# Optimization experiments

Hardware: AMD Instinct MI355X
Metric: run time of the kernel (lower is better)

Reference implementation:

```python
import jax, jax.numpy as jnp
import numpy as np

NUM_MID = 10   # hard-coded num_mid_nodes in HiPool.__init__
NUM_HIGH = 5   # ceil(10 / 2)


def map_low_to_high(num_low, num_high):
    # eye(num_high) repeat_interleaved by ceil(low/high) rows, truncated to num_low
    # == one-hot of i // edges_per_high
    edges_per_high = -(-num_low // num_high)
    return jax.nn.one_hot(jnp.arange(num_low) // edges_per_high, num_high,
                          dtype=jnp.float32)  # [low, high]


def cluster_attention(x, mapping, att):
    # x: [s, d], mapping: [s, m], att: [d, d]
    mid = mapping.T @ x                              # [m, d]
    scores = (mid @ att) @ x.T                       # [m, s]
    scores = scores * (1.0 - mapping).T              # zero (not -inf) own-cluster entries, as in source
    scores = jax.nn.softmax(scores, axis=1)
    return scores @ x + mid                          # [m, d]


def dense_gcn(x, adj, W, b):
    # torch_geometric DenseGCNConv with add_loop=True
    n = adj.shape[0]
    i = jnp.arange(n)
    adj = adj.at[i, i].set(1.0)
    deg = jnp.clip(jnp.sum(adj, axis=-1), 1.0, None) ** -0.5
    adj = deg[:, None] * adj * deg[None, :]
    return adj @ (x @ W) + b


def setup_inputs() -> dict:
    key = jax.random.key(0)
    ks = jax.random.split(key, 8)
    S, D, H = 8192, 768, 768
    return {
        "x": jax.random.normal(ks[0], (S, D), dtype=jnp.float32),
        "adjacency_matrix": jax.random.uniform(ks[1], (S, S), dtype=jnp.float32),
        "att_low_mid": jax.random.normal(ks[2], (D, D), dtype=jnp.float32) * 0.04,  # xavier_normal-ish
        "conv1_w": jax.random.normal(ks[3], (D, H), dtype=jnp.float32) * 0.04,
        "conv1_b": jnp.zeros((H,), dtype=jnp.float32),
        "att_mid_high": jax.random.normal(ks[4], (H, H), dtype=jnp.float32) * 0.04,
        "conv2_w": jax.random.normal(ks[5], (H, H), dtype=jnp.float32) * 0.04,
        "conv2_b": jnp.zeros((H,), dtype=jnp.float32),
    }


def reference(x, adjacency_matrix, att_low_mid, conv1_w, conv1_b,
              att_mid_high, conv2_w, conv2_b):
    s = x.shape[0]
    m1 = map_low_to_high(s, NUM_MID)                         # [s, 10]
    mid_adj = m1.T @ adjacency_matrix @ m1                   # [10, 10]
    mid_rep = cluster_attention(x, m1, att_low_mid)          # [10, d]
    x_mid = jax.nn.relu(dense_gcn(mid_rep, mid_adj, conv1_w, conv1_b))
    # F.dropout(...)[0]: dropout treated as identity (eval); [0] just dropped the batch dim
    m2 = map_low_to_high(NUM_MID, NUM_HIGH)                  # [10, 5]
    high_adj = m2.T @ mid_adj @ m2                           # [5, 5]
    high_rep = cluster_attention(x_mid, m2, att_mid_high)    # [5, h]
    out = jax.nn.relu(dense_gcn(high_rep, high_adj, conv2_w, conv2_b))
    return out.mean(axis=0)                                  # [h]
```

## Files before the change

### kernel.cpp

```cpp
#include <hip/hip_runtime.h>

constexpr int S    = 8192;
constexpr int D    = 768;
constexpr int NMID = 10;
constexpr int EPH  = 820;

constexpr int PART_ADJ = 0;
constexpr int PART_MID = 3200;
constexpr int OFF_ZB   = 64640;
constexpr int OFF_MATT = 64640;
constexpr int OFF_Y1   = 72320;
constexpr int OFF_Z2   = 80000;
constexpr int OFF_Y2   = 83840;
constexpr int ZERO_N   = 23040;
constexpr int OFF_MID  = 87680;
constexpr int OFF_XMID = 95360;
constexpr int OFF_SC   = 103040;
constexpr int OFF_SCB  = 184960;
constexpr int OFF_PVP  = 190080;

__device__ __forceinline__ void adj_partial(const float* __restrict__ A,
                                            float* __restrict__ ws, int item) {
    __shared__ float wred[4];
    int p = item >> 5, s = item & 31;
    int i = p / 10, j = p % 10;
    int r0 = i * EPH, nr = min(EPH, S - r0);
    int c0 = j * EPH, nc = min(EPH, S - c0);
    int rs0 = r0 + (nr * s) / 32, rs1 = r0 + (nr * (s + 1)) / 32;
    int nc4 = nc >> 2;
    int tid = threadIdx.x;
    float acc = 0.f;
    for (int r = rs0; r < rs1; ++r) {
        const float4* row = (const float4*)(A + (size_t)r * S + c0);
        if (tid < nc4) {
            float4 v = row[tid];
            acc += (v.x + v.y) + (v.z + v.w);
        }
    }
#pragma unroll
    for (int off = 32; off > 0; off >>= 1) acc += __shfl_down(acc, off, 64);
    int ln = tid & 63, wv = tid >> 6;
    if (ln == 0) wred[wv] = acc;
    __syncthreads();
    if (tid == 0) ws[PART_ADJ + item] = (wred[0] + wred[1]) + (wred[2] + wred[3]);
}

__device__ __forceinline__ void mid_partial(const float* __restrict__ x,
                                            float* __restrict__ ws, int item) {
    int cl = item / 24, rem = item % 24;
    int cc = rem >> 3, sp = rem & 7;
    int r0 = cl * EPH, nr = min(EPH, S - r0);
    int rs0 = r0 + (nr * sp) / 8, rs1 = r0 + (nr * (sp + 1)) / 8;
    int c = cc * 256 + threadIdx.x;
    float acc = 0.f;
    for (int r = rs0; r < rs1; ++r) acc += x[(size_t)r * D + c];
    ws[PART_MID + (sp * NMID + cl) * D + c] = acc;
}

template <int NR>
__device__ __forceinline__ void mm_core(const float* __restrict__ W,
                                        const float* mi,
                                        float* __restrict__ out, int kb) {
    int c = threadIdx.x;
    float a0[NR], a1[NR], a2[NR];
#pragma unroll
    for (int i = 0; i < NR; ++i) { a0[i] = 0.f; a1[i] = 0.f; a2[i] = 0.f; }
    for (int kk = 0; kk < 16; ++kk) {
        const float* wr = W + (size_t)(kb + kk) * D;
        float w0 = wr[c], w1 = wr[c + 256], w2 = wr[c + 512];
#pragma unroll
        for (int i = 0; i < NR; ++i) {
            float m = mi[i * 16 + kk];
            a0[i] += m * w0; a1[i] += m * w1; a2[i] += m * w2;
        }
    }
#pragma unroll
    for (int i = 0; i < NR; ++i) {
        atomicAdd(&out[i * D + c],       a0[i]);
        atomicAdd(&out[i * D + c + 256], a1[i]);
        atomicAdd(&out[i * D + c + 512], a2[i]);
    }
}

__global__ __launch_bounds__(256) void k1(const float* __restrict__ A,
                                          const float* __restrict__ x,
                                          float* __restrict__ ws) {
    int bx = blockIdx.x;
    if (bx < 800) adj_partial(A, ws, bx);
    else if (bx < 1040) mid_partial(x, ws, bx - 800);
    else {
        int b = bx - 1040;
        for (int t = b * 256 + threadIdx.x; t < ZERO_N; t += 16 * 256)
            ws[OFF_ZB + t] = 0.f;
    }
}

__global__ __launch_bounds__(256) void k2(const float* __restrict__ attL,
                                          const float* __restrict__ A,
                                          float* __restrict__ ws) {
    int bx = blockIdx.x;
    if (bx >= 48) { adj_partial(A, ws, 800 + bx - 48); return; }
    __shared__ float mi[160];
    int kb = bx * 16, tid = threadIdx.x;
    if (tid < 160) {
        int cl = tid >> 4, k = tid & 15;
        float s = 0.f;
#pragma unroll
        for (int sp = 0; sp < 8; ++sp)
            s += ws[PART_MID + (sp * NMID + cl) * D + kb + k];
        mi[tid] = s;
        ws[OFF_MID + cl * D + kb + k] = s;
    }
    __syncthreads();
    mm_core<10>(attL, mi, ws + OFF_MATT, kb);
}

__global__ __launch_bounds__(256) void k3(const float* __restrict__ x,
                                          const float* __restrict__ A,
                                          float* __restrict__ ws) {
    int bx = blockIdx.x;
    if (bx >= 256) { adj_partial(A, ws, 1600 + bx - 256); return; }
    __shared__ float ma[NMID * D];
    __shared__ float scl[32 * NMID];
    int tid = threadIdx.x;
    for (int t = tid; t < NMID * D; t += 256) ma[t] = ws[OFF_MATT + t];
    __syncthreads();
    const float4* maf = (const float4*)ma;
    const float4* x4  = (const float4*)x;
    int wave = tid >> 6, ln = tid & 63;
    int rbase = bx * 32 + wave * 8;
    for (int rr = 0; rr < 8; ++rr) {
        int r = rbase + rr;
        float4 v0 = x4[(size_t)r * 192 + ln];
        float4 v1 = x4[(size_t)r * 192 + 64 + ln];
        float4 v2 = x4[(size_t)r * 192 + 128 + ln];
        int rc = r / EPH;
#pragma unroll
        for (int i = 0; i < NMID; ++i) {
            float4 m0 = maf[i * 192 + ln];
            float4 m1 = maf[i * 192 + 64 + ln];
            float4 m2 = maf[i * 192 + 128 + ln];
            float p = m0.x * v0.x + m0.y * v0.y + m0.z * v0.z + m0.w * v0.w
                    + m1.x * v1.x + m1.y * v1.y + m1.z * v1.z + m1.w * v1.w
                    + m2.x * v2.x + m2.y * v2.y + m2.z * v2.z + m2.w * v2.w;
#pragma unroll
            for (int off = 32; off > 0; off >>= 1) p += __shfl_down(p, off, 64);
            if (ln == 0) {
                float v = (rc == i) ? 0.f : p;
                ws[OFF_SC + r * NMID + i] = v;
                scl[(wave * 8 + rr) * NMID + i] = v;
            }
        }
    }
    __syncthreads();
    if (tid < NMID) {
        float m = -1e30f;
        for (int r = 0; r < 32; ++r) m = fmaxf(m, scl[r * NMID + tid]);
        float s = 0.f;
        for (int r = 0; r < 32; ++r) s += expf(scl[r * NMID + tid] - m);
        ws[OFF_SCB + bx * 20 + tid * 2]     = m;
        ws[OFF_SCB + bx * 20 + tid * 2 + 1] = s;
    }
}

__global__ __launch_bounds__(256) void k4(const float* __restrict__ x,
                                          const float* __restrict__ A,
                                          float* __restrict__ ws) {
    int bx = blockIdx.x;
    if (bx >= 64) { adj_partial(A, ws, 2200 + bx - 64); return; }
    __shared__ float lm[160], ls[160], Mi[10], Inv[10], p[128 * NMID];
    int tid = threadIdx.x;
    if (tid < 160) {
        int i = tid >> 4, seg = tid & 15;
        float m = -1e30f;
        for (int b = seg * 16; b < seg * 16 + 16; ++b)
            m = fmaxf(m, ws[OFF_SCB + b * 20 + i * 2]);
        float s = 0.f;
        for (int b = seg * 16; b < seg * 16 + 16; ++b)
            s += ws[OFF_SCB + b * 20 + i * 2 + 1] *
                 expf(ws[OFF_SCB + b * 20 + i * 2] - m);
        lm[tid] = m; ls[tid] = s;
    }
    __syncthreads();
    if (tid < NMID) {
        float M = -1e30f;
        for (int g = 0; g < 16; ++g) M = fmaxf(M, lm[tid * 16 + g]);
        float Ssum = 0.f;
        for (int g = 0; g < 16; ++g) Ssum += ls[tid * 16 + g] * expf(lm[tid * 16 + g] - M);
        Mi[tid] = M; Inv[tid] = 1.f / Ssum;
    }
    __syncthreads();
    int r0 = bx * 128;
    for (int t = tid; t < 128 * NMID; t += 256) {
        int i = t % NMID;
        p[t] = expf(ws[OFF_SC + r0 * NMID + t] - Mi[i]) * Inv[i];
    }
    __syncthreads();
    float a0[NMID], a1[NMID], a2[NMID];
#pragma unroll
    for (int i = 0; i < NMID; ++i) { a0[i] = 0.f; a1[i] = 0.f; a2[i] = 0.f; }
    for (int r = 0; r < 128; ++r) {
        const float* xr = x + (size_t)(r0 + r) * D;
        float x0 = xr[tid], x1 = xr[tid + 256], x2 = xr[tid + 512];
#pragma unroll
        for (int i = 0; i < NMID; ++i) {
            float pv = p[r * NMID + i];
            a0[i] += pv * x0; a1[i] += pv * x1; a2[i] += pv * x2;
        }
    }
#pragma unroll
    for (int i = 0; i < NMID; ++i) {
        float* base = ws + OFF_PVP + (bx * NMID + i) * D;
        base[tid]       = a0[i];
        base[tid + 256] = a1[i];
        base[tid + 512] = a2[i];
    }
}

__global__ __launch_bounds__(256) void k5(const float* __restrict__ W1,
                                          const float* __restrict__ A,
                                          float* __restrict__ ws) {
    int bx = blockIdx.x;
    if (bx >= 48) { adj_partial(A, ws, 2800 + bx - 48); return; }
    __shared__ float mi[160];
    int kb = bx * 16, tid = threadIdx.x;
    if (tid < 160) {
        int cl = tid >> 4, k = tid & 15;
        float s = ws[OFF_MID + cl * D + kb + k];
        for (int b = 0; b < 64; ++b)
            s += ws[OFF_PVP + (b * NMID + cl) * D + kb + k];
        mi[tid] = s;
    }
    __syncthreads();
    mm_core<10>(W1, mi, ws + OFF_Y1, kb);
}

__global__ __launch_bounds__(256) void k6(const float* __restrict__ attH,
                                          const float* __restrict__ b1,
                                          float* __restrict__ ws) {
    __shared__ float aa[100], dg[10], NM[100], xml[160], mi[80];
    int tid = threadIdx.x;
    if (tid < 100) {
        float s = 0.f;
#pragma unroll
        for (int sp = 0; sp < 32; ++sp) s += ws[PART_ADJ + tid * 32 + sp];
        aa[tid] = s;
    }
    __syncthreads();
    if (tid < 10) {
        float s = 0.f;
#pragma unroll
        for (int j = 0; j < 10; ++j) s += (tid == j) ? 1.0f : aa[tid * 10 + j];
        dg[tid] = 1.0f / sqrtf(fmaxf(s, 1.0f));
    }
    __syncthreads();
    if (tid < 100) {
        int i = tid / 10, j = tid % 10;
        NM[tid] = dg[i] * ((i == j) ? 1.0f : aa[tid]) * dg[j];
    }
    __syncthreads();
    int kb = blockIdx.x * 16;
    if (tid < 160) {
        int i = tid >> 4, c = kb + (tid & 15);
        float s = b1[c];
#pragma unroll
        for (int j = 0; j < 10; ++j) s += NM[i * 10 + j] * ws[OFF_Y1 + j * D + c];
        float xm = fmaxf(s, 0.f);
        ws[OFF_XMID + i * D + c] = xm;
        xml[tid] = xm;
    }
    __syncthreads();
    if (tid < 80) {
        int a = tid >> 4, k = tid & 15;
        mi[tid] = xml[(2 * a) * 16 + k] + xml[(2 * a + 1) * 16 + k];
    }
    __syncthreads();
    mm_core<5>(attH, mi, ws + OFF_Z2, kb);
}

__global__ __launch_bounds__(256) void k7(const float* __restrict__ W2,
                                          float* __restrict__ ws) {
    __shared__ float s2[64], P2[50], mi[80];
    int tid = threadIdx.x, wv = tid >> 6, ln = tid & 63;
    for (int pp = wv; pp < 50; pp += 4) {
        int i = pp / 10, r = pp % 10;
        const float4* za = (const float4*)(ws + OFF_Z2 + i * D);
        const float4* xa = (const float4*)(ws + OFF_XMID + r * D);
        float acc = 0.f;
#pragma unroll
        for (int q = 0; q < 3; ++q) {
            float4 a = za[q * 64 + ln], b = xa[q * 64 + ln];
            acc += a.x * b.x + a.y * b.y + a.z * b.z + a.w * b.w;
        }
#pragma unroll
        for (int off = 32; off > 0; off >>= 1) acc += __shfl_down(acc, off, 64);
        if (ln == 0) s2[pp] = ((r >> 1) == i) ? 0.f : acc;
    }
    __syncthreads();
    if (tid < 5) {
        float mx = -1e30f;
#pragma unroll
        for (int r = 0; r < 10; ++r) mx = fmaxf(mx, s2[tid * 10 + r]);
        float sm = 0.f; float e[10];
#pragma unroll
        for (int r = 0; r < 10; ++r) { e[r] = expf(s2[tid * 10 + r] - mx); sm += e[r]; }
#pragma unroll
        for (int r = 0; r < 10; ++r) P2[tid * 10 + r] = e[r] / sm;
    }
    __syncthreads();
    int kb = blockIdx.x * 16;
    if (tid < 80) {
        int i = tid >> 4, c = kb + (tid & 15);
        float xm[10];
#pragma unroll
        for (int r = 0; r < 10; ++r) xm[r] = ws[OFF_XMID + r * D + c];
        float o = xm[2 * i] + xm[2 * i + 1];
#pragma unroll
        for (int r = 0; r < 10; ++r) o += P2[i * 10 + r] * xm[r];
        mi[tid] = o;
    }
    __syncthreads();
    mm_core<5>(W2, mi, ws + OFF_Y2, kb);
}

__global__ __launch_bounds__(768) void k8(const float* __restrict__ b2,
                                          const float* __restrict__ ws,
                                          float* __restrict__ out) {
    __shared__ float aa[100], ha[25], dh[5], NH[25];
    int tid = threadIdx.x;
    if (tid < 100) {
        float s = 0.f;
#pragma unroll
        for (int sp = 0; sp < 32; ++sp) s += ws[PART_ADJ + tid * 32 + sp];
        aa[tid] = s;
    }
    __syncthreads();
    if (tid < 25) {
        int a = tid / 5, b = tid % 5;
        ha[tid] = aa[(2 * a) * 10 + 2 * b] + aa[(2 * a) * 10 + 2 * b + 1]
                + aa[(2 * a + 1) * 10 + 2 * b] + aa[(2 * a + 1) * 10 + 2 * b + 1];
    }
    __syncthreads();
    if (tid < 5) {
        float s = 0.f;
#pragma unroll
        for (int j = 0; j < 5; ++j) s += (tid == j) ? 1.0f : ha[tid * 5 + j];
        dh[tid] = 1.0f / sqrtf(fmaxf(s, 1.0f));
    }
    __syncthreads();
    if (tid < 25) {
        int i = tid / 5, j = tid % 5;
        NH[tid] = dh[i] * ((i == j) ? 1.0f : ha[tid]) * dh[j];
    }
    __syncthreads();
    int c = tid;
    float y[5];
#pragma unroll
    for (int j = 0; j < 5; ++j) y[j] = ws[OFF_Y2 + j * D + c];
    float bias = b2[c];
    float s = 0.f;
#pragma unroll
    for (int i = 0; i < 5; ++i) {
        float v = bias;
#pragma unroll
        for (int j = 0; j < 5; ++j) v += NH[i * 5 + j] * y[j];
        s += fmaxf(v, 0.f);
    }
    out[c] = s * 0.2f;
}

extern "C" void kernel_launch(void* const* d_in, const int* in_sizes, int n_in,
                              void* d_out, int out_size, void* d_ws, size_t ws_size,
                              hipStream_t stream) {
    const float* x    = (const float*)d_in[0];
    const float* adj  = (const float*)d_in[1];
    const float* attL = (const float*)d_in[2];
    const float* W1   = (const float*)d_in[3];
    const float* b1   = (const float*)d_in[4];
    const float* attH = (const float*)d_in[5];
    const float* W2   = (const float*)d_in[6];
    const float* b2   = (const float*)d_in[7];
    float* ws  = (float*)d_ws;
    float* out = (float*)d_out;

    k1<<<1056, 256, 0, stream>>>(adj, x, ws);
    k2<<<848,  256, 0, stream>>>(attL, adj, ws);
    k3<<<856,  256, 0, stream>>>(x, adj, ws);
    k4<<<664,  256, 0, stream>>>(x, adj, ws);
    k5<<<448,  256, 0, stream>>>(W1, adj, ws);
    k6<<<48,   256, 0, stream>>>(attH, b1, ws);
    k7<<<48,   256, 0, stream>>>(W2, ws);
    k8<<<1,    768, 0, stream>>>(b2, ws, out);
}
```

Measured before the change: 160.1 us.

## Restructure pipeline: full-row adjacency reduction in first kernel, atomic-free matmul slices

The adjacency block-sum now runs as full-row reads in one persistent-grid first kernel, binned into 10 column clusters through shared memory, instead of being scattered across all later kernels. The small matmuls now compute full-K column slices with an in-block reduction in place of atomics into zeroed buffers. The attention-weighted sum uses atomics instead of per-block partials. The final GCN and mean are folded into the last kernel, dropping one launch. The aim is to read the 256MB adjacency with better coalescing and to cut launch and reduction overhead, at the cost of the adjacency pass no longer overlapping the later stages.

```diff
diff --git a/kernel.cpp b/kernel.cpp
--- a/kernel.cpp
+++ b/kernel.cpp
@@ -4,132 +4,166 @@
 constexpr int D    = 768;
 constexpr int NMID = 10;
 constexpr int EPH  = 820;
+constexpr int ASPLIT = 184;
+constexpr int MSPLIT = 20;
+constexpr int N_ADJ_IT = 10 * ASPLIT;
+constexpr int N_MID_IT = 10 * MSPLIT;
+constexpr int IT_ZERO  = N_ADJ_IT + N_MID_IT;
+constexpr int N_IT     = IT_ZERO + 1;
+constexpr int NB1 = 1024;
 
 constexpr int PART_ADJ = 0;
-constexpr int PART_MID = 3200;
-constexpr int OFF_ZB   = 64640;
-constexpr int OFF_MATT = 64640;
-constexpr int OFF_Y1   = 72320;
-constexpr int OFF_Z2   = 80000;
-constexpr int OFF_Y2   = 83840;
-constexpr int ZERO_N   = 23040;
-constexpr int OFF_MID  = 87680;
-constexpr int OFF_XMID = 95360;
-constexpr int OFF_SC   = 103040;
-constexpr int OFF_SCB  = 184960;
-constexpr int OFF_PVP  = 190080;
-
-__device__ __forceinline__ void adj_partial(const float* __restrict__ A,
-                                            float* __restrict__ ws, int item) {
-    __shared__ float wred[4];
-    int p = item >> 5, s = item & 31;
-    int i = p / 10, j = p % 10;
-    int r0 = i * EPH, nr = min(EPH, S - r0);
-    int c0 = j * EPH, nc = min(EPH, S - c0);
-    int rs0 = r0 + (nr * s) / 32, rs1 = r0 + (nr * (s + 1)) / 32;
-    int nc4 = nc >> 2;
+constexpr int PART_MID = 18432;
+constexpr int OFF_AA   = PART_MID + 153600;
+constexpr int OFF_MATT = 172160;
+constexpr int OFF_MREP = OFF_MATT + 7680;
+constexpr int OFF_XMID = OFF_MREP + 7680;
+constexpr int OFF_MID2 = OFF_XMID + 7680;
+constexpr int OFF_Z2   = OFF_MID2 + 3840;
+constexpr int OFF_SC   = OFF_Z2 + 3840;
+constexpr int OFF_SCB  = OFF_SC + 81920;
+
+template <int NR>
+__device__ __forceinline__ void fullk_slice(const float* __restrict__ W,
+                                            const float* inL, float* red,
+                                            float* outS, int c0) {
     int tid = threadIdx.x;
-    float acc = 0.f;
-    for (int r = rs0; r < rs1; ++r) {
-        const float4* row = (const float4*)(A + (size_t)r * S + c0);
-        if (tid < nc4) {
-            float4 v = row[tid];
-            acc += (v.x + v.y) + (v.z + v.w);
-        }
-    }
-#pragma unroll
-    for (int off = 32; off > 0; off >>= 1) acc += __shfl_down(acc, off, 64);
-    int ln = tid & 63, wv = tid >> 6;
-    if (ln == 0) wred[wv] = acc;
-    __syncthreads();
-    if (tid == 0) ws[PART_ADJ + item] = (wred[0] + wred[1]) + (wred[2] + wred[3]);
-}
-
-__device__ __forceinline__ void mid_partial(const float* __restrict__ x,
-                                            float* __restrict__ ws, int item) {
-    int cl = item / 24, rem = item % 24;
-    int cc = rem >> 3, sp = rem & 7;
-    int r0 = cl * EPH, nr = min(EPH, S - r0);
-    int rs0 = r0 + (nr * sp) / 8, rs1 = r0 + (nr * (sp + 1)) / 8;
-    int c = cc * 256 + threadIdx.x;
-    float acc = 0.f;
-    for (int r = rs0; r < rs1; ++r) acc += x[(size_t)r * D + c];
-    ws[PART_MID + (sp * NMID + cl) * D + c] = acc;
-}
-
-template <int NR>
-__device__ __forceinline__ void mm_core(const float* __restrict__ W,
-                                        const float* mi,
-                                        float* __restrict__ out, int kb) {
-    int c = threadIdx.x;
-    float a0[NR], a1[NR], a2[NR];
-#pragma unroll
-    for (int i = 0; i < NR; ++i) { a0[i] = 0.f; a1[i] = 0.f; a2[i] = 0.f; }
-    for (int kk = 0; kk < 16; ++kk) {
-        const float* wr = W + (size_t)(kb + kk) * D;
-        float w0 = wr[c], w1 = wr[c + 256], w2 = wr[c + 512];
-#pragma unroll
-        for (int i = 0; i < NR; ++i) {
-            float m = mi[i * 16 + kk];
-            a0[i] += m * w0; a1[i] += m * w1; a2[i] += m * w2;
-        }
-    }
-#pragma unroll
-    for (int i = 0; i < NR; ++i) {
-        atomicAdd(&out[i * D + c],       a0[i]);
-        atomicAdd(&out[i * D + c + 256], a1[i]);
-        atomicAdd(&out[i * D + c + 512], a2[i]);
-    }
+    int c = tid & 15, ks = tid >> 4;
+    float acc[NR];
+#pragma unroll
+    for (int i = 0; i < NR; ++i) acc[i] = 0.f;
+    int kb = ks * 48;
+    for (int kk = 0; kk < 48; ++kk) {
+        int k = kb + kk;
+        float w = W[(size_t)k * D + c0 + c];
+#pragma unroll
+        for (int i = 0; i < NR; ++i) acc[i] += inL[i * D + k] * w;
+    }
+#pragma unroll
+    for (int i = 0; i < NR; ++i) red[(ks * NR + i) * 16 + c] = acc[i];
+    __syncthreads();
+    if (tid < NR * 16) {
+        int i = tid >> 4, cc = tid & 15;
+        float s = 0.f;
+#pragma unroll
+        for (int k2 = 0; k2 < 16; ++k2) s += red[(k2 * NR + i) * 16 + cc];
+        outS[i * 16 + cc] = s;
+    }
+    __syncthreads();
 }
 
 __global__ __launch_bounds__(256) void k1(const float* __restrict__ A,
                                           const float* __restrict__ x,
                                           float* __restrict__ ws) {
-    int bx = blockIdx.x;
-    if (bx < 800) adj_partial(A, ws, bx);
-    else if (bx < 1040) mid_partial(x, ws, bx - 800);
-    else {
-        int b = bx - 1040;
-        for (int t = b * 256 + threadIdx.x; t < ZERO_N; t += 16 * 256)
-            ws[OFF_ZB + t] = 0.f;
+    __shared__ float bucket[2560];
+    __shared__ float red2[160];
+    int tid = threadIdx.x;
+    for (int it = blockIdx.x; it < N_IT; it += NB1) {
+        if (it < N_ADJ_IT) {
+            int i = it / ASPLIT, s = it % ASPLIT;
+            int r0 = i * EPH, nr = min(EPH, S - r0);
+            int rs0 = r0 + nr * s / ASPLIT, rs1 = r0 + nr * (s + 1) / ASPLIT;
+            float acc[8];
+#pragma unroll
+            for (int t = 0; t < 8; ++t) acc[t] = 0.f;
+            for (int r = rs0; r < rs1; ++r) {
+                const float4* row = (const float4*)(A + (size_t)r * S);
+#pragma unroll
+                for (int t = 0; t < 8; ++t) {
+                    float4 v = row[tid + 256 * t];
+                    acc[t] += (v.x + v.y) + (v.z + v.w);
+                }
+            }
+            for (int t = tid; t < 2560; t += 256) bucket[t] = 0.f;
+            __syncthreads();
+#pragma unroll
+            for (int t = 0; t < 8; ++t) {
+                int j = (tid + 256 * t) / 205;
+                bucket[j * 256 + tid] += acc[t];
+            }
+            __syncthreads();
+            if (tid < 160) {
+                int j = tid >> 4, seg = tid & 15;
+                float sm = 0.f;
+#pragma unroll
+                for (int u = 0; u < 16; ++u) sm += bucket[j * 256 + seg * 16 + u];
+                red2[tid] = sm;
+            }
+            __syncthreads();
+            if (tid < 10) {
+                float sm = 0.f;
+#pragma unroll
+                for (int g = 0; g < 16; ++g) sm += red2[tid * 16 + g];
+                ws[PART_ADJ + it * 10 + tid] = sm;
+            }
+            __syncthreads();
+        } else if (it < IT_ZERO) {
+            int m = it - N_ADJ_IT;
+            int cl = m / MSPLIT, sp = m % MSPLIT;
+            int r0 = cl * EPH, nr = min(EPH, S - r0);
+            int rs0 = r0 + nr * sp / MSPLIT, rs1 = r0 + nr * (sp + 1) / MSPLIT;
+            float a0 = 0.f, a1 = 0.f, a2 = 0.f;
+            for (int r = rs0; r < rs1; ++r) {
+                const float* xr = x + (size_t)r * D;
+                a0 += xr[tid]; a1 += xr[tid + 256]; a2 += xr[tid + 512];
+            }
+            int base = PART_MID + (sp * NMID + cl) * D;
+            ws[base + tid] = a0; ws[base + tid + 256] = a1; ws[base + tid + 512] = a2;
+        } else {
+            for (int t = tid; t < 7680; t += 256) ws[OFF_MREP + t] = 0.f;
+        }
     }
 }
 
 __global__ __launch_bounds__(256) void k2(const float* __restrict__ attL,
-                                          const float* __restrict__ A,
-                                          float* __restrict__ ws) {
-    int bx = blockIdx.x;
-    if (bx >= 48) { adj_partial(A, ws, 800 + bx - 48); return; }
-    __shared__ float mi[160];
-    int kb = bx * 16, tid = threadIdx.x;
-    if (tid < 160) {
-        int cl = tid >> 4, k = tid & 15;
-        float s = 0.f;
-#pragma unroll
-        for (int sp = 0; sp < 8; ++sp)
-            s += ws[PART_MID + (sp * NMID + cl) * D + kb + k];
-        mi[tid] = s;
-        ws[OFF_MID + cl * D + kb + k] = s;
-    }
-    __syncthreads();
-    mm_core<10>(attL, mi, ws + OFF_MATT, kb);
+                                          float* __restrict__ ws) {
+    int bx = blockIdx.x, tid = threadIdx.x;
+    if (bx < 48) {
+        __shared__ float midL[7680];
+        __shared__ float red[2560];
+        __shared__ float outS[160];
+        for (int t = tid; t < 7680; t += 256) {
+            int cl = t / D, k = t - cl * D;
+            float s = 0.f;
+#pragma unroll
+            for (int sp = 0; sp < MSPLIT; ++sp)
+                s += ws[PART_MID + (sp * NMID + cl) * D + k];
+            midL[t] = s;
+        }
+        __syncthreads();
+        fullk_slice<10>(attL, midL, red, outS, bx * 16);
+        if (tid < 160) ws[OFF_MATT + (tid >> 4) * D + bx * 16 + (tid & 15)] = outS[tid];
+    } else {
+        __shared__ float ared[200];
+        int base = (bx - 48) * 50;
+        if (tid < 200) {
+            int p = base + (tid >> 2), q = tid & 3;
+            int i = p / 10, j = p % 10;
+            float s = 0.f;
+            for (int t2 = q * 46; t2 < q * 46 + 46; ++t2)
+                s += ws[PART_ADJ + (i * ASPLIT + t2) * 10 + j];
+            ared[tid] = s;
+        }
+        __syncthreads();
+        if (tid < 50) {
+            int lb = (tid + base - base) * 4;
+            ws[OFF_AA + base + tid] = ared[lb] + ared[lb + 1] + ared[lb + 2] + ared[lb + 3];
+        }
+    }
 }
 
 __global__ __launch_bounds__(256) void k3(const float* __restrict__ x,
-                                          const float* __restrict__ A,
-                                          float* __restrict__ ws) {
-    int bx = blockIdx.x;
-    if (bx >= 256) { adj_partial(A, ws, 1600 + bx - 256); return; }
-    __shared__ float ma[NMID * D];
-    __shared__ float scl[32 * NMID];
-    int tid = threadIdx.x;
-    for (int t = tid; t < NMID * D; t += 256) ma[t] = ws[OFF_MATT + t];
+                                          float* __restrict__ ws) {
+    __shared__ float ma[7680];
+    __shared__ float scl[160];
+    int tid = threadIdx.x, bx = blockIdx.x;
+    for (int t = tid; t < 7680; t += 256) ma[t] = ws[OFF_MATT + t];
     __syncthreads();
     const float4* maf = (const float4*)ma;
     const float4* x4  = (const float4*)x;
     int wave = tid >> 6, ln = tid & 63;
-    int rbase = bx * 32 + wave * 8;
-    for (int rr = 0; rr < 8; ++rr) {
+    int rbase = bx * 16 + wave * 4;
+    for (int rr = 0; rr < 4; ++rr) {
         int r = rbase + rr;
         float4 v0 = x4[(size_t)r * 192 + ln];
         float4 v1 = x4[(size_t)r * 192 + 64 + ln];
@@ -148,35 +182,32 @@
             if (ln == 0) {
                 float v = (rc == i) ? 0.f : p;
                 ws[OFF_SC + r * NMID + i] = v;
-                scl[(wave * 8 + rr) * NMID + i] = v;
+                scl[(wave * 4 + rr) * NMID + i] = v;
             }
         }
     }
     __syncthreads();
     if (tid < NMID) {
         float m = -1e30f;
-        for (int r = 0; r < 32; ++r) m = fmaxf(m, scl[r * NMID + tid]);
-        float s = 0.f;
-        for (int r = 0; r < 32; ++r) s += expf(scl[r * NMID + tid] - m);
+        for (int r2 = 0; r2 < 16; ++r2) m = fmaxf(m, scl[r2 * NMID + tid]);
+        float s = 0.f;
+        for (int r2 = 0; r2 < 16; ++r2) s += expf(scl[r2 * NMID + tid] - m);
         ws[OFF_SCB + bx * 20 + tid * 2]     = m;
         ws[OFF_SCB + bx * 20 + tid * 2 + 1] = s;
     }
 }
 
 __global__ __launch_bounds__(256) void k4(const float* __restrict__ x,
-                                          const float* __restrict__ A,
-                                          float* __restrict__ ws) {
-    int bx = blockIdx.x;
-    if (bx >= 64) { adj_partial(A, ws, 2200 + bx - 64); return; }
-    __shared__ float lm[160], ls[160], Mi[10], Inv[10], p[128 * NMID];
-    int tid = threadIdx.x;
+                                          float* __restrict__ ws) {
+    __shared__ float lm[160], ls[160], Mi[10], Inv[10], p[640];
+    int tid = threadIdx.x, bx = blockIdx.x;
     if (tid < 160) {
         int i = tid >> 4, seg = tid & 15;
         float m = -1e30f;
-        for (int b = seg * 16; b < seg * 16 + 16; ++b)
+        for (int b = seg * 32; b < seg * 32 + 32; ++b)
             m = fmaxf(m, ws[OFF_SCB + b * 20 + i * 2]);
         float s = 0.f;
-        for (int b = seg * 16; b < seg * 16 + 16; ++b)
+        for (int b = seg * 32; b < seg * 32 + 32; ++b)
             s += ws[OFF_SCB + b * 20 + i * 2 + 1] *
                  expf(ws[OFF_SCB + b * 20 + i * 2] - m);
         lm[tid] = m; ls[tid] = s;
@@ -185,13 +216,13 @@
     if (tid < NMID) {
         float M = -1e30f;
         for (int g = 0; g < 16; ++g) M = fmaxf(M, lm[tid * 16 + g]);
-        float Ssum = 0.f;
-        for (int g = 0; g < 16; ++g) Ssum += ls[tid * 16 + g] * expf(lm[tid * 16 + g] - M);
-        Mi[tid] = M; Inv[tid] = 1.f / Ssum;
-    }
-    __syncthreads();
-    int r0 = bx * 128;
-    for (int t = tid; t < 128 * NMID; t += 256) {
+        float Ss = 0.f;
+        for (int g = 0; g < 16; ++g) Ss += ls[tid * 16 + g] * expf(lm[tid * 16 + g] - M);
+        Mi[tid] = M; Inv[tid] = 1.f / Ss;
+    }
+    __syncthreads();
+    int r0 = bx * 64;
+    for (int t = tid; t < 640; t += 256) {
         int i = t % NMID;
         p[t] = expf(ws[OFF_SC + r0 * NMID + t] - Mi[i]) * Inv[i];
     }
@@ -199,7 +230,7 @@
     float a0[NMID], a1[NMID], a2[NMID];
 #pragma unroll
     for (int i = 0; i < NMID; ++i) { a0[i] = 0.f; a1[i] = 0.f; a2[i] = 0.f; }
-    for (int r = 0; r < 128; ++r) {
+    for (int r = 0; r < 64; ++r) {
         const float* xr = x + (size_t)(r0 + r) * D;
         float x0 = xr[tid], x1 = xr[tid + 256], x2 = xr[tid + 512];
 #pragma unroll
@@ -210,163 +241,150 @@
     }
 #pragma unroll
     for (int i = 0; i < NMID; ++i) {
-        float* base = ws + OFF_PVP + (bx * NMID + i) * D;
-        base[tid]       = a0[i];
-        base[tid + 256] = a1[i];
-        base[tid + 512] = a2[i];
+        atomicAdd(&ws[OFF_MREP + i * D + tid],       a0[i]);
+        atomicAdd(&ws[OFF_MREP + i * D + tid + 256], a1[i]);
+        atomicAdd(&ws[OFF_MREP + i * D + tid + 512], a2[i]);
     }
 }
 
 __global__ __launch_bounds__(256) void k5(const float* __restrict__ W1,
-                                          const float* __restrict__ A,
-                                          float* __restrict__ ws) {
-    int bx = blockIdx.x;
-    if (bx >= 48) { adj_partial(A, ws, 2800 + bx - 48); return; }
-    __shared__ float mi[160];
-    int kb = bx * 16, tid = threadIdx.x;
-    if (tid < 160) {
-        int cl = tid >> 4, k = tid & 15;
-        float s = ws[OFF_MID + cl * D + kb + k];
-        for (int b = 0; b < 64; ++b)
-            s += ws[OFF_PVP + (b * NMID + cl) * D + kb + k];
-        mi[tid] = s;
-    }
-    __syncthreads();
-    mm_core<10>(W1, mi, ws + OFF_Y1, kb);
-}
-
-__global__ __launch_bounds__(256) void k6(const float* __restrict__ attH,
                                           const float* __restrict__ b1,
                                           float* __restrict__ ws) {
-    __shared__ float aa[100], dg[10], NM[100], xml[160], mi[80];
-    int tid = threadIdx.x;
-    if (tid < 100) {
-        float s = 0.f;
-#pragma unroll
-        for (int sp = 0; sp < 32; ++sp) s += ws[PART_ADJ + tid * 32 + sp];
-        aa[tid] = s;
-    }
-    __syncthreads();
+    __shared__ float inmid[7680];
+    __shared__ float red[2560];
+    __shared__ float Y1s[160];
+    __shared__ float aaL[100], dg[10], NM[100], xml[160];
+    int tid = threadIdx.x, c0 = blockIdx.x * 16;
+    for (int t = tid; t < 7680; t += 256) {
+        int cl = t / D, k = t - cl * D;
+        float s = ws[OFF_MREP + t];
+#pragma unroll
+        for (int sp = 0; sp < MSPLIT; ++sp)
+            s += ws[PART_MID + (sp * NMID + cl) * D + k];
+        inmid[t] = s;
+    }
+    if (tid < 100) aaL[tid] = ws[OFF_AA + tid];
+    __syncthreads();
+    fullk_slice<10>(W1, inmid, red, Y1s, c0);
     if (tid < 10) {
         float s = 0.f;
 #pragma unroll
-        for (int j = 0; j < 10; ++j) s += (tid == j) ? 1.0f : aa[tid * 10 + j];
-        dg[tid] = 1.0f / sqrtf(fmaxf(s, 1.0f));
+        for (int j = 0; j < 10; ++j) s += (tid == j) ? 1.f : aaL[tid * 10 + j];
+        dg[tid] = 1.f / sqrtf(fmaxf(s, 1.f));
     }
     __syncthreads();
     if (tid < 100) {
         int i = tid / 10, j = tid % 10;
-        NM[tid] = dg[i] * ((i == j) ? 1.0f : aa[tid]) * dg[j];
-    }
-    __syncthreads();
-    int kb = blockIdx.x * 16;
+        NM[tid] = dg[i] * ((i == j) ? 1.f : aaL[tid]) * dg[j];
+    }
+    __syncthreads();
     if (tid < 160) {
-        int i = tid >> 4, c = kb + (tid & 15);
-        float s = b1[c];
-#pragma unroll
-        for (int j = 0; j < 10; ++j) s += NM[i * 10 + j] * ws[OFF_Y1 + j * D + c];
-        float xm = fmaxf(s, 0.f);
-        ws[OFF_XMID + i * D + c] = xm;
+        int i = tid >> 4, cc = tid & 15;
+        float v = b1[c0 + cc];
+#pragma unroll
+        for (int j = 0; j < 10; ++j) v += NM[i * 10 + j] * Y1s[j * 16 + cc];
+        float xm = fmaxf(v, 0.f);
+        ws[OFF_XMID + i * D + c0 + cc] = xm;
         xml[tid] = xm;
     }
     __syncthreads();
     if (tid < 80) {
-        int a = tid >> 4, k = tid & 15;
-        mi[tid] = xml[(2 * a) * 16 + k] + xml[(2 * a + 1) * 16 + k];
-    }
-    __syncthreads();
-    mm_core<5>(attH, mi, ws + OFF_Z2, kb);
+        int a = tid >> 4, cc = tid & 15;
+        ws[OFF_MID2 + a * D + c0 + cc] = xml[(2 * a) * 16 + cc] + xml[(2 * a + 1) * 16 + cc];
+    }
+}
+
+__global__ __launch_bounds__(256) void k6(const float* __restrict__ attH,
+                                          float* __restrict__ ws) {
+    __shared__ float m2L[3840];
+    __shared__ float red[1280];
+    __shared__ float z2s[80];
+    int tid = threadIdx.x, c0 = blockIdx.x * 16;
+    for (int t = tid; t < 3840; t += 256) m2L[t] = ws[OFF_MID2 + t];
+    __syncthreads();
+    fullk_slice<5>(attH, m2L, red, z2s, c0);
+    if (tid < 80) ws[OFF_Z2 + (tid >> 4) * D + c0 + (tid & 15)] = z2s[tid];
 }
 
 __global__ __launch_bounds__(256) void k7(const float* __restrict__ W2,
-                                          float* __restrict__ ws) {
-    __shared__ float s2[64], P2[50], mi[80];
-    int tid = threadIdx.x, wv = tid >> 6, ln = tid & 63;
-    for (int pp = wv; pp < 50; pp += 4) {
+                                          const float* __restrict__ b2,
+                                          float* __restrict__ ws,
+                                          float* __restrict__ out) {
+    __shared__ float out2L[3840];
+    __shared__ float red[1280];
+    __shared__ float Y2s[80];
+    __shared__ float sred[200], s2[50], P2[50];
+    __shared__ float aaL[100], ha[25], dh[5], NH[25];
+    int tid = threadIdx.x, c0 = blockIdx.x * 16;
+    if (tid < 200) {
+        int pp = tid >> 2, q = tid & 3;
         int i = pp / 10, r = pp % 10;
-        const float4* za = (const float4*)(ws + OFF_Z2 + i * D);
-        const float4* xa = (const float4*)(ws + OFF_XMID + r * D);
-        float acc = 0.f;
-#pragma unroll
-        for (int q = 0; q < 3; ++q) {
-            float4 a = za[q * 64 + ln], b = xa[q * 64 + ln];
-            acc += a.x * b.x + a.y * b.y + a.z * b.z + a.w * b.w;
-        }
-#pragma unroll
-        for (int off = 32; off > 0; off >>= 1) acc += __shfl_down(acc, off, 64);
-        if (ln == 0) s2[pp] = ((r >> 1) == i) ? 0.f : acc;
+        const float* z  = ws + OFF_Z2 + i * D;
+        const float* xm = ws + OFF_XMID + r * D;
+        float s = 0.f;
+        for (int c = q * 192; c < q * 192 + 192; ++c) s += z[c] * xm[c];
+        sred[tid] = s;
+    }
+    if (tid < 100) aaL[tid] = ws[OFF_AA + tid];
+    __syncthreads();
+    if (tid < 50) {
+        int i = tid / 10, r = tid % 10;
+        float v = sred[tid * 4] + sred[tid * 4 + 1] + sred[tid * 4 + 2] + sred[tid * 4 + 3];
+        s2[tid] = ((r >> 1) == i) ? 0.f : v;
     }
     __syncthreads();
     if (tid < 5) {
         float mx = -1e30f;
 #pragma unroll
         for (int r = 0; r < 10; ++r) mx = fmaxf(mx, s2[tid * 10 + r]);
-        float sm = 0.f; float e[10];
+        float sm = 0.f;
+        float e[10];
 #pragma unroll
         for (int r = 0; r < 10; ++r) { e[r] = expf(s2[tid * 10 + r] - mx); sm += e[r]; }
 #pragma unroll
         for (int r = 0; r < 10; ++r) P2[tid * 10 + r] = e[r] / sm;
     }
     __syncthreads();
-    int kb = blockIdx.x * 16;
-    if (tid < 80) {
-        int i = tid >> 4, c = kb + (tid & 15);
-        float xm[10];
-#pragma unroll
-        for (int r = 0; r < 10; ++r) xm[r] = ws[OFF_XMID + r * D + c];
-        float o = xm[2 * i] + xm[2 * i + 1];
-#pragma unroll
-        for (int r = 0; r < 10; ++r) o += P2[i * 10 + r] * xm[r];
-        mi[tid] = o;
-    }
-    __syncthreads();
-    mm_core<5>(W2, mi, ws + OFF_Y2, kb);
-}
-
-__global__ __launch_bounds__(768) void k8(const float* __restrict__ b2,
-                                          const float* __restrict__ ws,
-                                          float* __restrict__ out) {
-    __shared__ float aa[100], ha[25], dh[5], NH[25];
-    int tid = threadIdx.x;
-    if (tid < 100) {
-        float s = 0.f;
-#pragma unroll
-        for (int sp = 0; sp < 32; ++sp) s += ws[PART_ADJ + tid * 32 + sp];
-        aa[tid] = s;
-    }
-    __syncthreads();
+    for (int t = tid; t < 3840; t += 256) {
+        int i = t / D, k = t - i * D;
+        float v = ws[OFF_MID2 + t];
+#pragma unroll
+        for (int r = 0; r < 10; ++r) v += P2[i * 10 + r] * ws[OFF_XMID + r * D + k];
+        out2L[t] = v;
+    }
+    __syncthreads();
+    fullk_slice<5>(W2, out2L, red, Y2s, c0);
     if (tid < 25) {
         int a = tid / 5, b = tid % 5;
-        ha[tid] = aa[(2 * a) * 10 + 2 * b] + aa[(2 * a) * 10 + 2 * b + 1]
-                + aa[(2 * a + 1) * 10 + 2 * b] + aa[(2 * a + 1) * 10 + 2 * b + 1];
+        ha[tid] = aaL[(2 * a) * 10 + 2 * b] + aaL[(2 * a) * 10 + 2 * b + 1]
+                + aaL[(2 * a + 1) * 10 + 2 * b] + aaL[(2 * a + 1) * 10 + 2 * b + 1];
     }
     __syncthreads();
     if (tid < 5) {
         float s = 0.f;
 #pragma unroll
-        for (int j = 0; j < 5; ++j) s += (tid == j) ? 1.0f : ha[tid * 5 + j];
-        dh[tid] = 1.0f / sqrtf(fmaxf(s, 1.0f));
+        for (int j = 0; j < 5; ++j) s += (tid == j) ? 1.f : ha[tid * 5 + j];
+        dh[tid] = 1.f / sqrtf(fmaxf(s, 1.f));
     }
     __syncthreads();
     if (tid < 25) {
         int i = tid / 5, j = tid % 5;
-        NH[tid] = dh[i] * ((i == j) ? 1.0f : ha[tid]) * dh[j];
-    }
-    __syncthreads();
-    int c = tid;
-    float y[5];
-#pragma unroll
-    for (int j = 0; j < 5; ++j) y[j] = ws[OFF_Y2 + j * D + c];
-    float bias = b2[c];
-    float s = 0.f;
-#pragma unroll
-    for (int i = 0; i < 5; ++i) {
-        float v = bias;
-#pragma unroll
-        for (int j = 0; j < 5; ++j) v += NH[i * 5 + j] * y[j];
-        s += fmaxf(v, 0.f);
-    }
-    out[c] = s * 0.2f;
+        NH[tid] = dh[i] * ((i == j) ? 1.f : ha[tid]) * dh[j];
+    }
+    __syncthreads();
+    if (tid < 16) {
+        int c = c0 + tid;
+        float bias = b2[c];
+        float s = 0.f;
+#pragma unroll
+        for (int i = 0; i < 5; ++i) {
+            float v = bias;
+#pragma unroll
+            for (int j = 0; j < 5; ++j) v += NH[i * 5 + j] * Y2s[j * 16 + tid];
+            s += fmaxf(v, 0.f);
+        }
+        out[c] = s * 0.2f;
+    }
 }
 
 extern "C" void kernel_launch(void* const* d_in, const int* in_sizes, int n_in,
@@ -383,12 +401,11 @@
     float* ws  = (float*)d_ws;
     float* out = (float*)d_out;
 
-    k1<<<1056, 256, 0, stream>>>(adj, x, ws);
-    k2<<<848,  256, 0, stream>>>(attL, adj, ws);
-    k3<<<856,  256, 0, stream>>>(x, adj, ws);
-    k4<<<664,  256, 0, stream>>>(x, adj, ws);
-    k5<<<448,  256, 0, stream>>>(W1, adj, ws);
-    k6<<<48,   256, 0, stream>>>(attH, b1, ws);
-    k7<<<48,   256, 0, stream>>>(W2, ws);
-    k8<<<1,    768, 0, stream>>>(b2, ws, out);
-}
+    k1<<<NB1, 256, 0, stream>>>(adj, x, ws);
+    k2<<<50,  256, 0, stream>>>(attL, ws);
+    k3<<<512, 256, 0, stream>>>(x, ws);
+    k4<<<128, 256, 0, stream>>>(x, ws);
+    k5<<<48,  256, 0, stream>>>(W1, b1, ws);
+    k6<<<48,  256, 0, stream>>>(attH, ws);
+    k7<<<48,  256, 0, stream>>>(W2, b2, ws, out);
+}
```

After: 193.8 us. 1.21x slower.
